# Kernel optimization log

Measured on AMD Instinct MI355X. Metric: run time of the kernel, lower is better.

## Reference

```python
import jax, jax.numpy as jnp
import numpy as np

N_NODES = 50000
N_EDGES = 800000
VOCAB = 1000
EMBED = 128
HIDDEN = 128
N_CLASSES = 10
N_GRAPHS = 64


def setup_inputs() -> dict:
    key = jax.random.key(0)
    ks = jax.random.split(key, 12)
    x_idx = jax.random.randint(ks[0], (N_NODES,), 0, VOCAB)
    edge_index = jax.random.randint(ks[1], (2, N_EDGES), 0, N_NODES)
    batch = jnp.sort(jax.random.randint(ks[2], (N_NODES,), 0, N_GRAPHS))
    s = lambda k, shp, fan: jax.random.normal(k, shp, jnp.float32) / jnp.sqrt(fan)
    return {
        "x_idx": x_idx,
        "edge_index": edge_index,
        "batch": batch,
        "embed_table": jax.random.normal(ks[3], (VOCAB, EMBED), jnp.float32),
        "Wl1": s(ks[4], (HIDDEN, EMBED), EMBED),
        "bl1": jnp.zeros((HIDDEN,), jnp.float32),
        "Wr1": s(ks[5], (HIDDEN, EMBED), EMBED),
        "Wl2": s(ks[6], (HIDDEN, HIDDEN), HIDDEN),
        "bl2": jnp.zeros((HIDDEN,), jnp.float32),
        "Wr2": s(ks[7], (HIDDEN, HIDDEN), HIDDEN),
        "linW": s(ks[8], (N_CLASSES, HIDDEN), HIDDEN),
        "linb": jnp.zeros((N_CLASSES,), jnp.float32),
    }


def _sage_conv(x, src, dst, Wl, bl, Wr):
    # mean aggregation of source features into destination nodes (PyG SAGEConv, aggr='mean')
    msg_sum = jax.ops.segment_sum(x[src], dst, num_segments=N_NODES)  # [N, d]
    cnt = jax.ops.segment_sum(jnp.ones((src.shape[0],), x.dtype), dst, num_segments=N_NODES)
    agg = msg_sum / jnp.maximum(cnt, 1.0)[:, None]
    # out = lin_l(agg) + lin_r(x); lin_l has bias, lin_r has none
    return agg @ Wl.T + bl + x @ Wr.T


def reference(x_idx, edge_index, batch, embed_table, Wl1, bl1, Wr1, Wl2, bl2, Wr2, linW, linb):
    src, dst = edge_index[0], edge_index[1]
    x = embed_table[x_idx]  # [N, EMBED]
    x = jax.nn.relu(_sage_conv(x, src, dst, Wl1, bl1, Wr1))
    x = jax.nn.relu(_sage_conv(x, src, dst, Wl2, bl2, Wr2))
    # global mean pool over graphs
    g_sum = jax.ops.segment_sum(x, batch, num_segments=N_GRAPHS)  # [G, HIDDEN]
    g_cnt = jax.ops.segment_sum(jnp.ones((x.shape[0],), x.dtype), batch, num_segments=N_GRAPHS)
    pooled = g_sum / jnp.maximum(g_cnt, 1.0)[:, None]
    return pooled @ linW.T + linb  # [G, N_CLASSES]
```

## Files before the change

kernel.cpp:

```cpp
#include <hip/hip_runtime.h>

#define N_NODES 50000
#define N_EDGES 800000
#define N_GRAPHS 64
#define SCAN_BLOCKS 196

#define NCHUNK 32
#define CHUNK_E (N_EDGES / NCHUNK)
#define NRANGE 4
#define RSZ (N_NODES / NRANGE)

#define K1_HIST (NCHUNK * NRANGE)
#define K1_EMBED (N_NODES * 16 / 256)
#define K1_PREP 32

typedef __bf16 bf16x8 __attribute__((ext_vector_type(8)));
typedef float f32x4 __attribute__((ext_vector_type(4)));

static __device__ __forceinline__ unsigned short f2bf(float f) {
    union { float f; unsigned u; } v; v.f = f;
    unsigned u = v.u;
    u += 0x7fffu + ((u >> 16) & 1u);
    return (unsigned short)(u >> 16);
}
static __device__ __forceinline__ float bf2f(unsigned short h) {
    union { unsigned u; float f; } v; v.u = ((unsigned)h) << 16; return v.f;
}
static __device__ __forceinline__ float bflo(unsigned w) {
    union { unsigned u; float f; } v; v.u = w << 16; return v.f;
}
static __device__ __forceinline__ float bfhi(unsigned w) {
    union { unsigned u; float f; } v; v.u = w & 0xffff0000u; return v.f;
}

__global__ __launch_bounds__(256) void k1_kernel(const int* __restrict__ dst,
                                                 int* __restrict__ part,
                                                 const int* __restrict__ x_idx,
                                                 const float* __restrict__ table,
                                                 unsigned short* __restrict__ X,
                                                 const float* __restrict__ Wl1,
                                                 const float* __restrict__ Wr1,
                                                 const float* __restrict__ Wl2,
                                                 const float* __restrict__ Wr2,
                                                 unsigned short* __restrict__ blob,
                                                 float* __restrict__ gsum) {
    const int b = blockIdx.x;
    if (b < K1_HIST) {
        __shared__ int h[RSZ];
        const int c = b >> 2;
        const int r = b & 3;
        const int rbase = r * RSZ;
        for (int i = threadIdx.x; i < RSZ; i += 256) h[i] = 0;
        __syncthreads();
        const int4* d4 = (const int4*)(dst + c * CHUNK_E);
        for (int i = threadIdx.x; i < CHUNK_E / 4; i += 256) {
            int4 d = d4[i];
            unsigned a;
            a = (unsigned)(d.x - rbase); if (a < RSZ) atomicAdd(&h[a], 1);
            a = (unsigned)(d.y - rbase); if (a < RSZ) atomicAdd(&h[a], 1);
            a = (unsigned)(d.z - rbase); if (a < RSZ) atomicAdd(&h[a], 1);
            a = (unsigned)(d.w - rbase); if (a < RSZ) atomicAdd(&h[a], 1);
        }
        __syncthreads();
        int* p = part + (size_t)c * N_NODES + rbase;
        for (int i = threadIdx.x; i < RSZ; i += 256) p[i] = h[i];
    } else if (b < K1_HIST + K1_EMBED) {
        int i = (b - K1_HIST) * 256 + threadIdx.x;
        int n = i >> 4, cq = i & 15;
        const float4* src = (const float4*)(table + (size_t)x_idx[n] * 128 + cq * 8);
        float4 a = src[0], bb = src[1];
        uint4 o;
        o.x = (unsigned)f2bf(a.x)  | ((unsigned)f2bf(a.y)  << 16);
        o.y = (unsigned)f2bf(a.z)  | ((unsigned)f2bf(a.w)  << 16);
        o.z = (unsigned)f2bf(bb.x) | ((unsigned)f2bf(bb.y) << 16);
        o.w = (unsigned)f2bf(bb.z) | ((unsigned)f2bf(bb.w) << 16);
        ((uint4*)X)[i] = o;
    } else {
        int s = (b - K1_HIST - K1_EMBED) * 256 + threadIdx.x;
        gsum[s] = 0.f;
        int g = s >> 12;
        int sl = s & 4095;
        int fidx = sl >> 6, lane = sl & 63;
        int m = fidx >> 5, kk = (fidx >> 3) & 3, tile = fidx & 7;
        const float* W = g ? (m ? Wr2 : Wl2) : (m ? Wr1 : Wl1);
        int n  = tile * 16 + (lane & 15);
        int k0 = kk * 32 + (lane >> 4) * 8;
        const float4* src = (const float4*)(W + n * 128 + k0);
        float4 a = src[0], bb = src[1];
        uint4 o;
        o.x = (unsigned)f2bf(a.x)  | ((unsigned)f2bf(a.y)  << 16);
        o.y = (unsigned)f2bf(a.z)  | ((unsigned)f2bf(a.w)  << 16);
        o.z = (unsigned)f2bf(bb.x) | ((unsigned)f2bf(bb.y) << 16);
        o.w = (unsigned)f2bf(bb.z) | ((unsigned)f2bf(bb.w) << 16);
        ((uint4*)blob)[s] = o;
    }
}

__global__ __launch_bounds__(256) void cntsum_kernel(const int* __restrict__ part,
                                                     int* __restrict__ cnt,
                                                     int* __restrict__ bsum) {
    int t = threadIdx.x;
    int n = blockIdx.x * 256 + t;
    int s = 0;
    if (n < N_NODES) {
#pragma unroll
        for (int c = 0; c < NCHUNK; ++c) s += part[(size_t)c * N_NODES + n];
        cnt[n] = s;
    }
#pragma unroll
    for (int off = 32; off > 0; off >>= 1) s += __shfl_down(s, off, 64);
    __shared__ int ws[4];
    if ((t & 63) == 0) ws[t >> 6] = s;
    __syncthreads();
    if (t == 0) bsum[blockIdx.x] = ws[0] + ws[1] + ws[2] + ws[3];
}

__global__ __launch_bounds__(256) void bscan_kernel(const int* __restrict__ bsum,
                                                    int* __restrict__ boff) {
    __shared__ int sd[256];
    int t = threadIdx.x;
    sd[t] = (t < SCAN_BLOCKS) ? bsum[t] : 0;
    __syncthreads();
    for (int off = 1; off < 256; off <<= 1) {
        int add = (t >= off) ? sd[t - off] : 0;
        __syncthreads();
        sd[t] += add;
        __syncthreads();
    }
    if (t < SCAN_BLOCKS) boff[t] = (t > 0) ? sd[t - 1] : 0;
}

__global__ __launch_bounds__(256) void rowptroff_kernel(const int* __restrict__ cnt,
                                                        const int* __restrict__ boff,
                                                        const int* __restrict__ part,
                                                        int* __restrict__ rowptr,
                                                        int* __restrict__ off) {
    __shared__ int sd[256];
    int t = threadIdx.x;
    int i = blockIdx.x * 256 + t;
    int v = (i < N_NODES) ? cnt[i] : 0;
    sd[t] = v;
    __syncthreads();
    for (int o = 1; o < 256; o <<= 1) {
        int add = (t >= o) ? sd[t - o] : 0;
        __syncthreads();
        sd[t] += add;
        __syncthreads();
    }
    int excl = sd[t] - v + boff[blockIdx.x];
    if (i < N_NODES) {
        rowptr[i] = excl;
        if (i == N_NODES - 1) rowptr[N_NODES] = excl + v;
        int run = excl;
#pragma unroll
        for (int c = 0; c < NCHUNK; ++c) {
            off[(size_t)c * N_NODES + i] = run;
            run += part[(size_t)c * N_NODES + i];
        }
    }
}

__global__ __launch_bounds__(256) void scatter_kernel(const int* __restrict__ src,
                                                      const int* __restrict__ dst,
                                                      const int* __restrict__ off,
                                                      int* __restrict__ csr) {
    __shared__ int h[RSZ];
    const int c = blockIdx.x >> 2;
    const int r = blockIdx.x & 3;
    const int rbase = r * RSZ;
    const int* o = off + (size_t)c * N_NODES + rbase;
    for (int i = threadIdx.x; i < RSZ; i += 256) h[i] = o[i];
    __syncthreads();
    const int4* d4 = (const int4*)(dst + c * CHUNK_E);
    const int4* s4 = (const int4*)(src + c * CHUNK_E);
    for (int i = threadIdx.x; i < CHUNK_E / 4; i += 256) {
        int4 d = d4[i];
        int4 s = s4[i];
        unsigned a;
        a = (unsigned)(d.x - rbase); if (a < RSZ) csr[atomicAdd(&h[a], 1)] = s.x;
        a = (unsigned)(d.y - rbase); if (a < RSZ) csr[atomicAdd(&h[a], 1)] = s.y;
        a = (unsigned)(d.z - rbase); if (a < RSZ) csr[atomicAdd(&h[a], 1)] = s.z;
        a = (unsigned)(d.w - rbase); if (a < RSZ) csr[atomicAdd(&h[a], 1)] = s.w;
    }
}

__global__ __launch_bounds__(256) void agg_kernel(const unsigned short* __restrict__ X,
                                                  const int* __restrict__ rowptr,
                                                  const int* __restrict__ csr,
                                                  unsigned short* __restrict__ AGG) {
    int wid  = (blockIdx.x * 256 + threadIdx.x) >> 6;
    int lane = threadIdx.x & 63;
    if (wid >= N_NODES) return;
    int beg = rowptr[wid], end = rowptr[wid + 1];
    const unsigned* Xw = (const unsigned*)X;
    float sx = 0.f, sy = 0.f;
    int i = beg;
    for (; i + 8 <= end; i += 8) {
        unsigned v0 = Xw[(size_t)csr[i + 0] * 64 + lane];
        unsigned v1 = Xw[(size_t)csr[i + 1] * 64 + lane];
        unsigned v2 = Xw[(size_t)csr[i + 2] * 64 + lane];
        unsigned v3 = Xw[(size_t)csr[i + 3] * 64 + lane];
        unsigned v4 = Xw[(size_t)csr[i + 4] * 64 + lane];
        unsigned v5 = Xw[(size_t)csr[i + 5] * 64 + lane];
        unsigned v6 = Xw[(size_t)csr[i + 6] * 64 + lane];
        unsigned v7 = Xw[(size_t)csr[i + 7] * 64 + lane];
        sx += ((bflo(v0) + bflo(v1)) + (bflo(v2) + bflo(v3))) +
              ((bflo(v4) + bflo(v5)) + (bflo(v6) + bflo(v7)));
        sy += ((bfhi(v0) + bfhi(v1)) + (bfhi(v2) + bfhi(v3))) +
              ((bfhi(v4) + bfhi(v5)) + (bfhi(v6) + bfhi(v7)));
    }
    for (; i < end; ++i) {
        unsigned v = Xw[(size_t)csr[i] * 64 + lane];
        sx += bflo(v); sy += bfhi(v);
    }
    float inv = 1.f / (float)max(end - beg, 1);
    ((unsigned*)AGG)[(size_t)wid * 64 + lane] =
        (unsigned)f2bf(sx * inv) | ((unsigned)f2bf(sy * inv) << 16);
}

__global__ __launch_bounds__(256) void gemm_kernel(const unsigned short* __restrict__ A0,
                                                   const unsigned short* __restrict__ A1,
                                                   const unsigned short* __restrict__ wblob,
                                                   const float* __restrict__ bias,
                                                   unsigned short* __restrict__ Y) {
    __shared__ char lds[65536];
    const int t = threadIdx.x, lane = t & 63, w = t >> 6;
    const int row0 = blockIdx.x * 128 + w * 32;

    {
        const char* src = (const char*)wblob + w * 16384 + lane * 16;
        char* dst = lds + w * 16384;
#pragma unroll
        for (int i = 0; i < 16; ++i) {
            __builtin_amdgcn_global_load_lds(
                (const __attribute__((address_space(1))) unsigned*)(src + i * 1024),
                (__attribute__((address_space(3))) unsigned*)(dst + i * 1024), 16, 0, 0);
        }
    }
    __syncthreads();

    f32x4 acc[2][8];
#pragma unroll
    for (int rt = 0; rt < 2; ++rt)
#pragma unroll
        for (int tl = 0; tl < 8; ++tl) acc[rt][tl] = (f32x4){0.f, 0.f, 0.f, 0.f};

    int rA = min(row0 + (lane & 15),      N_NODES - 1);
    int rB = min(row0 + 16 + (lane & 15), N_NODES - 1);
    const int kl = (lane >> 4) * 8;

#pragma unroll
    for (int km = 0; km < 8; ++km) {
        const unsigned short* A = (km < 4) ? A0 : A1;
        int k0 = (km & 3) * 32 + kl;
        bf16x8 a0 = *(const bf16x8*)(A + (size_t)rA * 128 + k0);
        bf16x8 a1 = *(const bf16x8*)(A + (size_t)rB * 128 + k0);
        const char* bbase = lds + km * 8192 + lane * 16;
#pragma unroll
        for (int tile = 0; tile < 8; ++tile) {
            bf16x8 b = *(const bf16x8*)(bbase + tile * 1024);
            acc[0][tile] = __builtin_amdgcn_mfma_f32_16x16x32_bf16(a0, b, acc[0][tile], 0, 0, 0);
            acc[1][tile] = __builtin_amdgcn_mfma_f32_16x16x32_bf16(a1, b, acc[1][tile], 0, 0, 0);
        }
    }

    const int c     = lane & 15;
    const int rbase = (lane >> 4) * 4;
#pragma unroll
    for (int rt = 0; rt < 2; ++rt) {
#pragma unroll
        for (int tile = 0; tile < 8; ++tile) {
            int col = tile * 16 + c;
            float bv = bias[col];
#pragma unroll
            for (int j = 0; j < 4; ++j) {
                int r = row0 + rt * 16 + rbase + j;
                if (r < N_NODES)
                    Y[(size_t)r * 128 + col] = f2bf(fmaxf(acc[rt][tile][j] + bv, 0.f));
            }
        }
    }
}

__global__ __launch_bounds__(256) void gemm_pool_kernel(const unsigned short* __restrict__ A0,
                                                        const unsigned short* __restrict__ A1,
                                                        const unsigned short* __restrict__ wblob,
                                                        const float* __restrict__ bias,
                                                        const int* __restrict__ batch,
                                                        float* __restrict__ gsum) {
    __shared__ char lds[65536];
    const int t = threadIdx.x, lane = t & 63, w = t >> 6;
    const int brow0 = blockIdx.x * 128;
    const int row0  = brow0 + w * 32;

    {
        const char* src = (const char*)wblob + w * 16384 + lane * 16;
        char* dst = lds + w * 16384;
#pragma unroll
        for (int i = 0; i < 16; ++i) {
            __builtin_amdgcn_global_load_lds(
                (const __attribute__((address_space(1))) unsigned*)(src + i * 1024),
                (__attribute__((address_space(3))) unsigned*)(dst + i * 1024), 16, 0, 0);
        }
    }
    __syncthreads();

    f32x4 acc[2][8];
#pragma unroll
    for (int rt = 0; rt < 2; ++rt)
#pragma unroll
        for (int tl = 0; tl < 8; ++tl) acc[rt][tl] = (f32x4){0.f, 0.f, 0.f, 0.f};

    int rA = min(row0 + (lane & 15),      N_NODES - 1);
    int rB = min(row0 + 16 + (lane & 15), N_NODES - 1);
    const int kl = (lane >> 4) * 8;

#pragma unroll
    for (int km = 0; km < 8; ++km) {
        const unsigned short* A = (km < 4) ? A0 : A1;
        int k0 = (km & 3) * 32 + kl;
        bf16x8 a0 = *(const bf16x8*)(A + (size_t)rA * 128 + k0);
        bf16x8 a1 = *(const bf16x8*)(A + (size_t)rB * 128 + k0);
        const char* bbase = lds + km * 8192 + lane * 16;
#pragma unroll
        for (int tile = 0; tile < 8; ++tile) {
            bf16x8 b = *(const bf16x8*)(bbase + tile * 1024);
            acc[0][tile] = __builtin_amdgcn_mfma_f32_16x16x32_bf16(a0, b, acc[0][tile], 0, 0, 0);
            acc[1][tile] = __builtin_amdgcn_mfma_f32_16x16x32_bf16(a1, b, acc[1][tile], 0, 0, 0);
        }
    }

    __syncthreads();
    float* ftile = (float*)lds;
    const int c     = lane & 15;
    const int rbase = (lane >> 4) * 4;
#pragma unroll
    for (int rt = 0; rt < 2; ++rt) {
#pragma unroll
        for (int tile = 0; tile < 8; ++tile) {
            int col = tile * 16 + c;
            float bv = bias[col];
#pragma unroll
            for (int j = 0; j < 4; ++j) {
                int lr = w * 32 + rt * 16 + rbase + j;
                ftile[lr * 128 + col] = fmaxf(acc[rt][tile][j] + bv, 0.f);
            }
        }
    }
    __syncthreads();

    const int col  = t & 127;
    const int half = t >> 7;
    float s = 0.f;
    int curg = -1;
    for (int rr = 0; rr < 64; ++rr) {
        int r = brow0 + half * 64 + rr;
        if (r >= N_NODES) break;
        int g = batch[r];
        if (g != curg) {
            if (curg >= 0) atomicAdd(&gsum[curg * 128 + col], s);
            curg = g; s = 0.f;
        }
        s += ftile[(half * 64 + rr) * 128 + col];
    }
    if (curg >= 0) atomicAdd(&gsum[curg * 128 + col], s);
}

__global__ void final_kernel(const float* __restrict__ gsum, const int* __restrict__ batch,
                             const float* __restrict__ linW, const float* __restrict__ linb,
                             float* __restrict__ out) {
    int t = blockIdx.x * 256 + threadIdx.x;
    if (t >= N_GRAPHS * 10) return;
    int g = t / 10, j = t % 10;
    int bnd[2];
    for (int c = 0; c < 2; ++c) {
        int target = g + c;
        int lo = 0, hi = N_NODES;
        while (lo < hi) { int mid = (lo + hi) >> 1; if (batch[mid] < target) lo = mid + 1; else hi = mid; }
        bnd[c] = lo;
    }
    float invc = 1.f / (float)max(bnd[1] - bnd[0], 1);
    float s = 0.f;
    for (int k = 0; k < 128; ++k) s += gsum[g * 128 + k] * linW[j * 128 + k];
    out[t] = linb[j] + s * invc;
}

extern "C" void kernel_launch(void* const* d_in, const int* in_sizes, int n_in,
                              void* d_out, int out_size, void* d_ws, size_t ws_size,
                              hipStream_t stream) {
    const int*   x_idx = (const int*)d_in[0];
    const int*   eidx  = (const int*)d_in[1];
    const int*   batch = (const int*)d_in[2];
    const float* table = (const float*)d_in[3];
    const float* Wl1   = (const float*)d_in[4];
    const float* bl1   = (const float*)d_in[5];
    const float* Wr1   = (const float*)d_in[6];
    const float* Wl2   = (const float*)d_in[7];
    const float* bl2   = (const float*)d_in[8];
    const float* Wr2   = (const float*)d_in[9];
    const float* linW  = (const float*)d_in[10];
    const float* linb  = (const float*)d_in[11];
    float*       out   = (float*)d_out;

    const int* src = eidx;
    const int* dst = eidx + N_EDGES;

    unsigned short* X    = (unsigned short*)d_ws;
    unsigned short* AGG  = X   + (size_t)N_NODES * 128;
    unsigned short* Y1   = AGG + (size_t)N_NODES * 128;
    unsigned short* blob = Y1  + (size_t)N_NODES * 128;
    float* gsum = (float*)(blob + 65536);
    int* cnt    = (int*)(gsum + N_GRAPHS * 128);
    int* rowptr = cnt + N_NODES;
    int* csr    = rowptr + (N_NODES + 1);
    int* bsum   = csr + N_EDGES;
    int* boff   = bsum + SCAN_BLOCKS;
    int* part   = boff + SCAN_BLOCKS;
    int* off    = part + (size_t)NCHUNK * N_NODES;

    k1_kernel<<<K1_HIST + K1_EMBED + K1_PREP, 256, 0, stream>>>(
        dst, part, x_idx, table, X, Wl1, Wr1, Wl2, Wr2, blob, gsum);
    cntsum_kernel   <<<SCAN_BLOCKS, 256, 0, stream>>>(part, cnt, bsum);
    bscan_kernel    <<<1, 256, 0, stream>>>(bsum, boff);
    rowptroff_kernel<<<SCAN_BLOCKS, 256, 0, stream>>>(cnt, boff, part, rowptr, off);
    scatter_kernel  <<<NCHUNK * NRANGE, 256, 0, stream>>>(src, dst, off, csr);

    agg_kernel <<<dim3(N_NODES * 64 / 256), 256, 0, stream>>>(X, rowptr, csr, AGG);
    gemm_kernel<<<dim3((N_NODES + 127) / 128), 256, 0, stream>>>(AGG, X, blob, bl1, Y1);
    agg_kernel      <<<dim3(N_NODES * 64 / 256), 256, 0, stream>>>(Y1, rowptr, csr, AGG);
    gemm_pool_kernel<<<dim3((N_NODES + 127) / 128), 256, 0, stream>>>(AGG, Y1, blob + 32768, bl2, batch, gsum);

    final_kernel<<<3, 256, 0, stream>>>(gsum, batch, linW, linb, out);
}
```

Measured before the change: 171.6 us.

## Split node features into four 32-column quarter planes for cache-friendly gathers

Node feature matrices (X, Y1, AGG) are stored as four separate planes of 32 bf16 columns each. The aggregation kernel runs over a second grid dimension, one plane at a time, with 16 lanes per node. The intent is to shrink the gathered working set per pass so random source-row gathers hit L2/MALL more often. The GEMM loads and stores are remapped to the new layout. The separate single-block block-offset scan kernel is also folded into rowptroff, which now rescans bsum redundantly in every block to save a launch. The cost is more, smaller 64-byte gathers and re-reading rowptr/csr four times.

New measurement: 179.7 us. 1.05x slower.

```diff
diff --git a/kernel.cpp b/kernel.cpp
--- a/kernel.cpp
+++ b/kernel.cpp
@@ -13,6 +13,9 @@
 #define K1_HIST (NCHUNK * NRANGE)
 #define K1_EMBED (N_NODES * 16 / 256)
 #define K1_PREP 32
+
+#define QDW (N_NODES * 16)
+#define QUS (N_NODES * 32)
 
 typedef __bf16 bf16x8 __attribute__((ext_vector_type(8)));
 typedef float f32x4 __attribute__((ext_vector_type(4)));
@@ -74,7 +77,8 @@
         o.y = (unsigned)f2bf(a.z)  | ((unsigned)f2bf(a.w)  << 16);
         o.z = (unsigned)f2bf(bb.x) | ((unsigned)f2bf(bb.y) << 16);
         o.w = (unsigned)f2bf(bb.z) | ((unsigned)f2bf(bb.w) << 16);
-        ((uint4*)X)[i] = o;
+        int qq = cq >> 2;
+        ((uint4*)X)[(size_t)qq * (N_NODES * 4) + n * 4 + (cq & 3)] = o;
     } else {
         int s = (b - K1_HIST - K1_EMBED) * 256 + threadIdx.x;
         gsum[s] = 0.f;
@@ -115,28 +119,24 @@
     if (t == 0) bsum[blockIdx.x] = ws[0] + ws[1] + ws[2] + ws[3];
 }
 
-__global__ __launch_bounds__(256) void bscan_kernel(const int* __restrict__ bsum,
-                                                    int* __restrict__ boff) {
-    __shared__ int sd[256];
-    int t = threadIdx.x;
-    sd[t] = (t < SCAN_BLOCKS) ? bsum[t] : 0;
-    __syncthreads();
-    for (int off = 1; off < 256; off <<= 1) {
-        int add = (t >= off) ? sd[t - off] : 0;
-        __syncthreads();
-        sd[t] += add;
-        __syncthreads();
-    }
-    if (t < SCAN_BLOCKS) boff[t] = (t > 0) ? sd[t - 1] : 0;
-}
-
 __global__ __launch_bounds__(256) void rowptroff_kernel(const int* __restrict__ cnt,
-                                                        const int* __restrict__ boff,
+                                                        const int* __restrict__ bsum,
                                                         const int* __restrict__ part,
                                                         int* __restrict__ rowptr,
                                                         int* __restrict__ off) {
+    __shared__ int sb[256];
     __shared__ int sd[256];
     int t = threadIdx.x;
+    sb[t] = (t < SCAN_BLOCKS) ? bsum[t] : 0;
+    __syncthreads();
+    for (int o = 1; o < 256; o <<= 1) {
+        int add = (t >= o) ? sb[t - o] : 0;
+        __syncthreads();
+        sb[t] += add;
+        __syncthreads();
+    }
+    int boff = (blockIdx.x > 0) ? sb[blockIdx.x - 1] : 0;
+
     int i = blockIdx.x * 256 + t;
     int v = (i < N_NODES) ? cnt[i] : 0;
     sd[t] = v;
@@ -147,7 +147,7 @@
         sd[t] += add;
         __syncthreads();
     }
-    int excl = sd[t] - v + boff[blockIdx.x];
+    int excl = sd[t] - v + boff;
     if (i < N_NODES) {
         rowptr[i] = excl;
         if (i == N_NODES - 1) rowptr[N_NODES] = excl + v;
@@ -184,37 +184,34 @@
     }
 }
 
-__global__ __launch_bounds__(256) void agg_kernel(const unsigned short* __restrict__ X,
+__global__ __launch_bounds__(256) void agg_kernel(const unsigned* __restrict__ Xq,
                                                   const int* __restrict__ rowptr,
                                                   const int* __restrict__ csr,
-                                                  unsigned short* __restrict__ AGG) {
-    int wid  = (blockIdx.x * 256 + threadIdx.x) >> 6;
-    int lane = threadIdx.x & 63;
-    if (wid >= N_NODES) return;
-    int beg = rowptr[wid], end = rowptr[wid + 1];
-    const unsigned* Xw = (const unsigned*)X;
+                                                  unsigned* __restrict__ AGGq) {
+    const int t = threadIdx.x;
+    const int lane = t & 63;
+    const int g = lane >> 4;
+    const int f = lane & 15;
+    const int n = blockIdx.x * 16 + (t >> 6) * 4 + g;
+    const unsigned* Xb = Xq + (size_t)blockIdx.y * QDW;
+    int beg = rowptr[n], end = rowptr[n + 1];
     float sx = 0.f, sy = 0.f;
     int i = beg;
-    for (; i + 8 <= end; i += 8) {
-        unsigned v0 = Xw[(size_t)csr[i + 0] * 64 + lane];
-        unsigned v1 = Xw[(size_t)csr[i + 1] * 64 + lane];
-        unsigned v2 = Xw[(size_t)csr[i + 2] * 64 + lane];
-        unsigned v3 = Xw[(size_t)csr[i + 3] * 64 + lane];
-        unsigned v4 = Xw[(size_t)csr[i + 4] * 64 + lane];
-        unsigned v5 = Xw[(size_t)csr[i + 5] * 64 + lane];
-        unsigned v6 = Xw[(size_t)csr[i + 6] * 64 + lane];
-        unsigned v7 = Xw[(size_t)csr[i + 7] * 64 + lane];
-        sx += ((bflo(v0) + bflo(v1)) + (bflo(v2) + bflo(v3))) +
-              ((bflo(v4) + bflo(v5)) + (bflo(v6) + bflo(v7)));
-        sy += ((bfhi(v0) + bfhi(v1)) + (bfhi(v2) + bfhi(v3))) +
-              ((bfhi(v4) + bfhi(v5)) + (bfhi(v6) + bfhi(v7)));
+    for (; i + 4 <= end; i += 4) {
+        int s0 = csr[i], s1 = csr[i + 1], s2 = csr[i + 2], s3 = csr[i + 3];
+        unsigned v0 = Xb[(size_t)s0 * 16 + f];
+        unsigned v1 = Xb[(size_t)s1 * 16 + f];
+        unsigned v2 = Xb[(size_t)s2 * 16 + f];
+        unsigned v3 = Xb[(size_t)s3 * 16 + f];
+        sx += (bflo(v0) + bflo(v1)) + (bflo(v2) + bflo(v3));
+        sy += (bfhi(v0) + bfhi(v1)) + (bfhi(v2) + bfhi(v3));
     }
     for (; i < end; ++i) {
-        unsigned v = Xw[(size_t)csr[i] * 64 + lane];
+        unsigned v = Xb[(size_t)csr[i] * 16 + f];
         sx += bflo(v); sy += bfhi(v);
     }
     float inv = 1.f / (float)max(end - beg, 1);
-    ((unsigned*)AGG)[(size_t)wid * 64 + lane] =
+    AGGq[(size_t)blockIdx.y * QDW + (size_t)n * 16 + f] =
         (unsigned)f2bf(sx * inv) | ((unsigned)f2bf(sy * inv) << 16);
 }
 
@@ -251,10 +248,9 @@
 
 #pragma unroll
     for (int km = 0; km < 8; ++km) {
-        const unsigned short* A = (km < 4) ? A0 : A1;
-        int k0 = (km & 3) * 32 + kl;
-        bf16x8 a0 = *(const bf16x8*)(A + (size_t)rA * 128 + k0);
-        bf16x8 a1 = *(const bf16x8*)(A + (size_t)rB * 128 + k0);
+        const unsigned short* Aq = ((km < 4) ? A0 : A1) + (size_t)(km & 3) * QUS;
+        bf16x8 a0 = *(const bf16x8*)(Aq + (size_t)rA * 32 + kl);
+        bf16x8 a1 = *(const bf16x8*)(Aq + (size_t)rB * 32 + kl);
         const char* bbase = lds + km * 8192 + lane * 16;
 #pragma unroll
         for (int tile = 0; tile < 8; ++tile) {
@@ -272,11 +268,13 @@
         for (int tile = 0; tile < 8; ++tile) {
             int col = tile * 16 + c;
             float bv = bias[col];
+            int q = col >> 5, wc = col & 31;
 #pragma unroll
             for (int j = 0; j < 4; ++j) {
                 int r = row0 + rt * 16 + rbase + j;
                 if (r < N_NODES)
-                    Y[(size_t)r * 128 + col] = f2bf(fmaxf(acc[rt][tile][j] + bv, 0.f));
+                    Y[(size_t)q * QUS + (size_t)r * 32 + wc] =
+                        f2bf(fmaxf(acc[rt][tile][j] + bv, 0.f));
             }
         }
     }
@@ -317,10 +315,9 @@
 
 #pragma unroll
     for (int km = 0; km < 8; ++km) {
-        const unsigned short* A = (km < 4) ? A0 : A1;
-        int k0 = (km & 3) * 32 + kl;
-        bf16x8 a0 = *(const bf16x8*)(A + (size_t)rA * 128 + k0);
-        bf16x8 a1 = *(const bf16x8*)(A + (size_t)rB * 128 + k0);
+        const unsigned short* Aq = ((km < 4) ? A0 : A1) + (size_t)(km & 3) * QUS;
+        bf16x8 a0 = *(const bf16x8*)(Aq + (size_t)rA * 32 + kl);
+        bf16x8 a1 = *(const bf16x8*)(Aq + (size_t)rB * 32 + kl);
         const char* bbase = lds + km * 8192 + lane * 16;
 #pragma unroll
         for (int tile = 0; tile < 8; ++tile) {
@@ -414,20 +411,18 @@
     int* rowptr = cnt + N_NODES;
     int* csr    = rowptr + (N_NODES + 1);
     int* bsum   = csr + N_EDGES;
-    int* boff   = bsum + SCAN_BLOCKS;
-    int* part   = boff + SCAN_BLOCKS;
+    int* part   = bsum + SCAN_BLOCKS;
     int* off    = part + (size_t)NCHUNK * N_NODES;
 
     k1_kernel<<<K1_HIST + K1_EMBED + K1_PREP, 256, 0, stream>>>(
         dst, part, x_idx, table, X, Wl1, Wr1, Wl2, Wr2, blob, gsum);
     cntsum_kernel   <<<SCAN_BLOCKS, 256, 0, stream>>>(part, cnt, bsum);
-    bscan_kernel    <<<1, 256, 0, stream>>>(bsum, boff);
-    rowptroff_kernel<<<SCAN_BLOCKS, 256, 0, stream>>>(cnt, boff, part, rowptr, off);
+    rowptroff_kernel<<<SCAN_BLOCKS, 256, 0, stream>>>(cnt, bsum, part, rowptr, off);
     scatter_kernel  <<<NCHUNK * NRANGE, 256, 0, stream>>>(src, dst, off, csr);
 
-    agg_kernel <<<dim3(N_NODES * 64 / 256), 256, 0, stream>>>(X, rowptr, csr, AGG);
+    agg_kernel <<<dim3(N_NODES / 16, 4), 256, 0, stream>>>((const unsigned*)X, rowptr, csr, (unsigned*)AGG);
     gemm_kernel<<<dim3((N_NODES + 127) / 128), 256, 0, stream>>>(AGG, X, blob, bl1, Y1);
-    agg_kernel      <<<dim3(N_NODES * 64 / 256), 256, 0, stream>>>(Y1, rowptr, csr, AGG);
+    agg_kernel      <<<dim3(N_NODES / 16, 4), 256, 0, stream>>>((const unsigned*)Y1, rowptr, csr, (unsigned*)AGG);
     gemm_pool_kernel<<<dim3((N_NODES + 127) / 128), 256, 0, stream>>>(AGG, Y1, blob + 32768, bl2, batch, gsum);
 
     final_kernel<<<3, 256, 0, stream>>>(gsum, batch, linW, linb, out);
```
